# Performance work log

Hardware: AMD Instinct MI355X
Metric: run time of the kernel (lower is better)

Reference implementation:

```python
import jax, jax.numpy as jnp
import numpy as np

B, N_IN, N_OPS, E = 2048, 64, 1024, 64   # graphs, leaf inputs, operations, embed_size
N_OIO, N_TIO, VOCAB = 4, 4, 1000         # one-input ops, two-input ops, embedding rows


def setup_inputs() -> dict:
    key = jax.random.key(0)
    ks = jax.random.split(key, 8)
    rng = np.random.default_rng(0)
    # random valid DAG topology: op j may read any node with index < N_IN + j
    op_kind = rng.integers(0, 2, N_OPS)
    t_oio = rng.integers(0, N_OIO, N_OPS)
    t_tio = rng.integers(0, N_TIO, N_OPS)
    op_w_idx = np.where(op_kind == 0, t_oio, N_OIO + t_tio).astype(np.int32)
    op_in1 = np.array([rng.integers(0, N_IN + j) for j in range(N_OPS)], dtype=np.int32)
    op_in2 = np.array([rng.integers(0, N_IN + j) for j in range(N_OPS)], dtype=np.int32)
    s = 0.1  # keep relu chain numerically tame
    return {
        "input_ids": jax.random.randint(ks[0], (B, N_IN), 0, VOCAB, dtype=jnp.int32),
        "op_w_idx": jnp.asarray(op_w_idx),
        "op_in1": jnp.asarray(op_in1),
        "op_in2": jnp.asarray(op_in2),
        "embedding": jax.random.normal(ks[1], (VOCAB, E), jnp.float32) * s,
        "oio_W": jax.random.normal(ks[2], (N_OIO, E, E), jnp.float32) * s,
        "oio_b": jax.random.normal(ks[3], (N_OIO, E), jnp.float32) * s,
        "tio_W": jax.random.normal(ks[4], (N_TIO, 2 * E, E), jnp.float32) * s,
        "tio_b": jax.random.normal(ks[5], (N_TIO, E), jnp.float32) * s,
        "final_W": jax.random.normal(ks[6], (E, 1), jnp.float32) * s,
        "final_b": jax.random.normal(ks[7], (1,), jnp.float32) * s,
    }


def reference(input_ids, op_w_idx, op_in1, op_in2, embedding,
              oio_W, oio_b, tio_W, tio_b, final_W, final_b):
    # Unify weights: one-input Linear(E,E) padded with zeros on the x2 half,
    # so cat(x1, x2) @ W_pad + b == x1 @ W + b (identical math to the torch module).
    W_all = jnp.concatenate(
        [jnp.concatenate([oio_W, jnp.zeros_like(oio_W)], axis=1), tio_W], axis=0)  # (8, 2E, E)
    b_all = jnp.concatenate([oio_b, tio_b], axis=0)                                # (8, E)

    leaves = embedding[input_ids]                                   # (B, N_IN, E)
    nodes0 = jnp.concatenate(
        [leaves, jnp.zeros((B, N_OPS, E), leaves.dtype)], axis=1)   # (B, N_IN+N_OPS, E)

    def step(nodes, op):
        j, widx, i1, i2 = op
        x1 = jnp.take(nodes, i1, axis=1)                            # (B, E)
        x2 = jnp.take(nodes, i2, axis=1)                            # (B, E)
        h = jax.nn.relu(jnp.concatenate([x1, x2], axis=-1) @ W_all[widx] + b_all[widx])
        nodes = jax.lax.dynamic_update_slice(nodes, h[:, None, :], (0, N_IN + j, 0))
        return nodes, None

    xs = (jnp.arange(N_OPS, dtype=jnp.int32), op_w_idx, op_in1, op_in2)
    nodes, _ = jax.lax.scan(step, nodes0, xs)

    # operation_counter: final Linear(E, 1) on the last produced node tensor
    return nodes[:, -1, :] @ final_W + final_b                      # (B, 1)
```

## Files before the change

### kernel.cpp

```cpp
#include <hip/hip_runtime.h>

#define NIN 64
#define NOPS 1024
#define NB 2048
#define NNODES 1088
#define SLAB_SH 18

#define WS_SCHED 0u
#define WS_LEV   8192u
#define WS_WT    16384u
#define WS_BIAS  147456u
#define WS_NODES 163840u

#define LM_LINES 0u
#define LM_SCHED 65536u
#define LM_MSTA  73728u
#define LM_TOTAL 77824u

typedef unsigned int u32;
typedef unsigned short u16;
typedef unsigned long long u64;
typedef _Float16 f16;
typedef _Float16 f16x8 __attribute__((ext_vector_type(8)));
typedef _Float16 f16x4 __attribute__((ext_vector_type(4)));
typedef float f32x4 __attribute__((ext_vector_type(4)));

#define MFMA16(a, b, c) __builtin_amdgcn_mfma_f32_16x16x32_f16((a), (b), (c), 0, 0, 0)


__global__ __launch_bounds__(1024) void k_sched(const int* __restrict__ wxv,
                                                const int* __restrict__ in1v,
                                                const int* __restrict__ in2v,
                                                char* __restrict__ ws, int cap) {
  __shared__ int s1[NOPS], s2[NOPS], sw[NOPS], slv[NOPS];
  __shared__ int lcnt[132];
  __shared__ int cnt2[1032];
  __shared__ u64 s_pack[NOPS];
  __shared__ int dl[NNODES], slot_of[NNODES], stk[NNODES];
  __shared__ int opPos[NOPS];
  __shared__ unsigned char needG[NOPS];
  __shared__ int s_flag, s_nlev, s_top, s_next;
  const int j = threadIdx.x;
  s1[j] = in1v[j]; s2[j] = in2v[j]; sw[j] = wxv[j]; slv[j] = 1;
  needG[j] = 0;
  if (j < 132) lcnt[j] = 0;
  if (j < 1032) cnt2[j] = 0;
  __syncthreads();
  for (int it = 0; it < NOPS + 1; ++it) {
    if (j == 0) s_flag = 0;
    __syncthreads();
    int p1 = s1[j];
    int l1 = (p1 >= NIN) ? slv[p1 - NIN] : 0;
    int l2 = 0;
    if (sw[j] >= 4) { int p2 = s2[j]; l2 = (p2 >= NIN) ? slv[p2 - NIN] : 0; }
    int nl = 1 + (l1 > l2 ? l1 : l2);
    if (nl != slv[j]) { slv[j] = nl; s_flag = 1; }
    __syncthreads();
    int f = s_flag;
    __syncthreads();
    if (!f) break;
  }
  if (j == 0) s_nlev = 0;
  __syncthreads();
  atomicMax(&s_nlev, slv[j]);
  __syncthreads();
  u32* wl = (u32*)(ws + WS_LEV);
  const int nlev = s_nlev;
  if (nlev > 127) { if (j == 0) { wl[0] = 0; wl[1] = 0; wl[2] = 1; } return; }
  atomicAdd(&lcnt[slv[j]], 1);
  atomicAdd(&cnt2[slv[j] * 8 + sw[j]], 1);
  __syncthreads();
  if (j == 0) {
    int acc = 0;
    for (int L = 1; L <= nlev; ++L) { int c = lcnt[L]; lcnt[L] = acc; acc += c; }
  }
  __syncthreads();
  int base = -1;
  if (j >= 8 && j < (nlev + 1) * 8) {
    int L = j >> 3, mm = j & 7;
    int s = lcnt[L];
    for (int q = 0; q < mm; ++q) s += cnt2[L * 8 + q];
    base = s;
  }
  u16* msta = (u16*)(ws + WS_LEV + 4096);
  for (int t = j; t < 2048; t += 1024) msta[t] = (u16)NOPS;
  __syncthreads();
  if (base >= 0) { cnt2[j] = base; msta[j] = (u16)base; }
  __syncthreads();
  { int slot = atomicAdd(&cnt2[slv[j] * 8 + sw[j]], 1);
    u64 p = (u64)(u32)s1[j] | ((u64)(u32)s2[j] << 11) | ((u64)(u32)sw[j] << 22) | ((u64)(u32)j << 25);
    s_pack[slot] = p;
    opPos[j] = slot - lcnt[slv[j]]; }
  __syncthreads();
  if (j == NOPS - 1) needG[j] = 1;
  { int L = slv[j];
    int i1n = s1[j];
    if (i1n >= NIN) { int p = i1n - NIN; if (!(slv[p] == L - 1 && opPos[p] < 64)) needG[p] = 1; }
    if (sw[j] >= 4) {
      int i2n = s2[j];
      if (i2n >= NIN) { int p = i2n - NIN; if (!(slv[p] == L - 1 && opPos[p] < 64)) needG[p] = 1; }
    } }
  for (int t = j; t < NNODES; t += 1024) dl[t] = (t < NIN) ? 0 : slv[t - NIN];
  __syncthreads();
  atomicMax(&dl[s1[j]], slv[j]);
  if (sw[j] >= 4) atomicMax(&dl[s2[j]], slv[j]);
  __syncthreads();
  if (j == 0) { dl[NNODES - 1] = nlev + 1; s_top = 0; s_next = NIN; }
  if (j < NIN) slot_of[j] = j;
  __syncthreads();
  for (int L = 1; L <= nlev; ++L) {
    for (int t = j; t < NNODES; t += 1024)
      if (dl[t] == L - 1) { int p = atomicAdd(&s_top, 1); stk[p] = slot_of[t]; }
    __syncthreads();
    if (slv[j] == L) {
      int p = atomicSub(&s_top, 1);
      int s;
      if (p >= 1) s = stk[p - 1]; else s = atomicAdd(&s_next, 1);
      slot_of[NIN + j] = s;
    }
    __syncthreads();
    if (j == 0 && s_top < 0) s_top = 0;
    __syncthreads();
  }
  {
    u64 m = s_pack[j];
    int i1n = (int)(m & 2047u), i2n = (int)((m >> 11) & 2047u);
    u32 wxn = (u32)((m >> 22) & 7u);
    int opn = (int)((m >> 25) & 2047u);
    int Lop = slv[opn];
    int two = (wxn >= 4);
    if (!two) i2n = i1n;
    u32 f1 = 0, p1 = 0, f2 = 0, p2 = 0;
    if (i1n >= NIN) { int p = i1n - NIN;
      if (slv[p] == Lop - 1 && opPos[p] < 64) { f1 = 1; p1 = (u32)opPos[p]; } }
    if (i2n >= NIN) { int p = i2n - NIN;
      if (slv[p] == Lop - 1 && opPos[p] < 64) { f2 = 1; p2 = (u32)opPos[p]; } }
    u32 op_pos = (u32)opPos[opn];
    u32 ldsout = (op_pos < 64) ? 1u : 0u;
    u32 gout   = needG[opn] ? 1u : 0u;
    u32 s1slot = (u32)slot_of[i1n];
    u32 s2slot = (u32)slot_of[i2n];
    u64 nm = (u64)s1slot | ((u64)s2slot << 11) | ((u64)wxn << 22)
           | ((u64)(u32)slot_of[NIN + opn] << 25)
           | ((u64)p1 << 36) | ((u64)f1 << 43)
           | ((u64)p2 << 44) | ((u64)f2 << 51)
           | ((u64)(op_pos & 63u) << 52) | ((u64)ldsout << 59)
           | ((u64)gout << 60);
    ((u64*)(ws + WS_SCHED))[j] = nm;
  }
  if (j == 0) {
    wl[0] = (u32)nlev;
    wl[1] = (u32)slot_of[NNODES - 1];
    wl[2] = (s_next > cap) ? 1u : 0u;
  }
}

__global__ __launch_bounds__(256) void k_weights(const float* __restrict__ oW,
                                                 const float* __restrict__ ob,
                                                 const float* __restrict__ tW,
                                                 const float* __restrict__ tb,
                                                 char* __restrict__ ws) {
  f16* wt = (f16*)(ws + WS_WT);
  int t = blockIdx.x * 256 + threadIdx.x;
  #pragma unroll
  for (int q = 0; q < 4; ++q) {
    int e = t * 4 + q;
    int mat = e >> 13, n = (e >> 7) & 63, k = e & 127;
    float v;
    if (mat < 4) v = (k < 64) ? oW[mat * 4096 + k * 64 + n] : 0.f;
    else         v = tW[(mat - 4) * 8192 + k * 64 + n];
    wt[e] = (f16)v;
  }
  if (blockIdx.x == 0) {
    float* bs = (float*)(ws + WS_BIAS);
    for (int q = threadIdx.x; q < 512; q += 256)
      bs[q] = (q < 256) ? ob[q] : tb[q - 256];
  }
}

__global__ __launch_bounds__(256) void k_leaves(const int* __restrict__ ids,
                                                const float* __restrict__ emb,
                                                char* __restrict__ ws) {
  int p = blockIdx.x * 256 + threadIdx.x;
  int i = p >> 11, b = p & 2047;
  int id = ids[b * 64 + i];
  const f32x4* src = (const f32x4*)(emb + (u32)id * 64u);
  f16x8* dst = (f16x8*)(ws + WS_NODES + ((u32)i << SLAB_SH) + (u32)b * 128u);
  #pragma unroll
  for (int q = 0; q < 8; ++q) {
    f32x4 lo = src[2 * q], hi = src[2 * q + 1];
    f16x8 v = { (f16)lo.x, (f16)lo.y, (f16)lo.z, (f16)lo.w,
                (f16)hi.x, (f16)hi.y, (f16)hi.z, (f16)hi.w };
    dst[q] = v;
  }
}

__global__ __launch_bounds__(512, 4) void k_main(char* __restrict__ ws) {
  extern __shared__ char lds[];
  const int tid = threadIdx.x;
  const u32* wl = (const u32*)(ws + WS_LEV);
  if (wl[2]) return;
  for (int t = tid; t < NOPS; t += 512)
    ((u64*)(lds + LM_SCHED))[t] = ((const u64*)(ws + WS_SCHED))[t];
  for (int t = tid; t < 1024; t += 512)
    ((u32*)(lds + LM_MSTA))[t] = ((const u32*)(ws + WS_LEV + 4096))[t];
  const int nlev = (int)wl[0];

  const int lane   = tid & 63;
  const int m      = tid >> 6;
  const int lhi    = lane >> 4, llo = lane & 15;
  const int op_sub = llo >> 2;
  const int brow   = llo & 3;
  const int r0     = blockIdx.x * 4;
  char* nodes = ws + WS_NODES;

  const f16* wp = (const f16*)(ws + WS_WT) + m * 8192 + llo * 128 + lhi * 8;
  const f16x8 W00 = *(const f16x8*)(wp +        0), W01 = *(const f16x8*)(wp +       32),
              W10 = *(const f16x8*)(wp + 2048 + 0), W11 = *(const f16x8*)(wp + 2048 + 32),
              W20 = *(const f16x8*)(wp + 4096 + 0), W21 = *(const f16x8*)(wp + 4096 + 32),
              W30 = *(const f16x8*)(wp + 6144 + 0), W31 = *(const f16x8*)(wp + 6144 + 32);
  f16x8 W02 = {}, W03 = {}, W12 = {}, W13 = {}, W22 = {}, W23 = {}, W32 = {}, W33 = {};
  if (m >= 4) {
    W02 = *(const f16x8*)(wp +        64); W03 = *(const f16x8*)(wp +        96);
    W12 = *(const f16x8*)(wp + 2048 + 64); W13 = *(const f16x8*)(wp + 2048 + 96);
    W22 = *(const f16x8*)(wp + 4096 + 64); W23 = *(const f16x8*)(wp + 4096 + 96);
    W32 = *(const f16x8*)(wp + 6144 + 64); W33 = *(const f16x8*)(wp + 6144 + 96);
  }
  const float* bsp = (const float*)(ws + WS_BIAS) + m * 64 + lhi * 4;
  const f32x4 B0 = *(const f32x4*)(bsp),      B1 = *(const f32x4*)(bsp + 16),
              B2 = *(const f32x4*)(bsp + 32), B3 = *(const f32x4*)(bsp + 48);
  __syncthreads();

  const u64* s_sched = (const u64*)(lds + LM_SCHED);
  const u16* s_msta  = (const u16*)(lds + LM_MSTA);

  const u32 a_off  = (u32)((r0 + brow) * 128 + lhi * 16);
  const u32 st_off = (u32)((r0 + brow) * 128 + lhi * 8);
  const u32 key   = (u32)(brow << 4);
  const u32 aL0   = (u32)(brow * 128 + ((lhi * 16)      ^ key));
  const u32 aL1   = (u32)(brow * 128 + ((lhi * 16 + 64) ^ key));
  const u32 stL0  = (u32)(brow * 128 + ((      lhi * 8) ^ key));
  const u32 stL1  = (u32)(brow * 128 + (( 32 + lhi * 8) ^ key));
  const u32 stL2  = (u32)(brow * 128 + (( 64 + lhi * 8) ^ key));
  const u32 stL3  = (u32)(brow * 128 + (( 96 + lhi * 8) ^ key));

  for (int L = 1; L <= nlev; ++L) {
    const u32 rb = (u32)(((L - 1) & 1) << 15);
    const u32 wb = (u32)((L & 1) << 15);
    int k0 = (int)s_msta[L * 8 + m];
    int k1 = (int)s_msta[L * 8 + m + 1];
    k0 = __builtin_amdgcn_readfirstlane(k0);
    k1 = __builtin_amdgcn_readfirstlane(k1);
    const int ke = k1 - 1;
    for (int g = k0; g < k1; g += 4) {
      int kop = g + op_sub; kop = kop > ke ? ke : kop;
      u64 md = s_sched[kop];
      f16x8 a0, a1;
      if ((md >> 43) & 1) {
        const char* l1 = lds + rb + (((u32)(md >> 36) & 63u) << 9);
        a0 = *(const f16x8*)(l1 + aL0);
        a1 = *(const f16x8*)(l1 + aL1);
      } else {
        const char* b1 = nodes + ((u64)((u32)md & 2047u) << SLAB_SH) + a_off;
        a0 = *(const f16x8*)(b1);
        a1 = *(const f16x8*)(b1 + 64);
      }
      f16x8 a2 = {}, a3 = {};
      if (m >= 4) {
        if ((md >> 51) & 1) {
          const char* l2 = lds + rb + (((u32)(md >> 44) & 63u) << 9);
          a2 = *(const f16x8*)(l2 + aL0);
          a3 = *(const f16x8*)(l2 + aL1);
        } else {
          const char* b2 = nodes + ((u64)(((u32)(md >> 11)) & 2047u) << SLAB_SH) + a_off;
          a2 = *(const f16x8*)(b2);
          a3 = *(const f16x8*)(b2 + 64);
        }
      }
      f32x4 c0 = B0, c1 = B1, c2 = B2, c3 = B3;
      __builtin_amdgcn_s_setprio(1);
      c0 = MFMA16(W00, a0, c0); c0 = MFMA16(W01, a1, c0);
      c1 = MFMA16(W10, a0, c1); c1 = MFMA16(W11, a1, c1);
      c2 = MFMA16(W20, a0, c2); c2 = MFMA16(W21, a1, c2);
      c3 = MFMA16(W30, a0, c3); c3 = MFMA16(W31, a1, c3);
      if (m >= 4) {
        c0 = MFMA16(W02, a2, c0); c0 = MFMA16(W03, a3, c0);
        c1 = MFMA16(W12, a2, c1); c1 = MFMA16(W13, a3, c1);
        c2 = MFMA16(W22, a2, c2); c2 = MFMA16(W23, a3, c2);
        c3 = MFMA16(W32, a2, c3); c3 = MFMA16(W33, a3, c3);
      }
      __builtin_amdgcn_s_setprio(0);
      f16x4 r0v = { (f16)(c0.x > 0.f ? c0.x : 0.f), (f16)(c0.y > 0.f ? c0.y : 0.f),
                    (f16)(c0.z > 0.f ? c0.z : 0.f), (f16)(c0.w > 0.f ? c0.w : 0.f) };
      f16x4 r1v = { (f16)(c1.x > 0.f ? c1.x : 0.f), (f16)(c1.y > 0.f ? c1.y : 0.f),
                    (f16)(c1.z > 0.f ? c1.z : 0.f), (f16)(c1.w > 0.f ? c1.w : 0.f) };
      f16x4 r2v = { (f16)(c2.x > 0.f ? c2.x : 0.f), (f16)(c2.y > 0.f ? c2.y : 0.f),
                    (f16)(c2.z > 0.f ? c2.z : 0.f), (f16)(c2.w > 0.f ? c2.w : 0.f) };
      f16x4 r3v = { (f16)(c3.x > 0.f ? c3.x : 0.f), (f16)(c3.y > 0.f ? c3.y : 0.f),
                    (f16)(c3.z > 0.f ? c3.z : 0.f), (f16)(c3.w > 0.f ? c3.w : 0.f) };
      if ((md >> 59) & 1) {
        char* lp = lds + wb + (((u32)(md >> 52) & 63u) << 9);
        *(f16x4*)(lp + stL0) = r0v;
        *(f16x4*)(lp + stL1) = r1v;
        *(f16x4*)(lp + stL2) = r2v;
        *(f16x4*)(lp + stL3) = r3v;
      }
      if ((md >> 60) & 1) {
        char* st = nodes + (((u64)((md >> 25) & 2047u)) << SLAB_SH) + st_off;
        *(f16x4*)(st)      = r0v;
        *(f16x4*)(st + 32) = r1v;
        *(f16x4*)(st + 64) = r2v;
        *(f16x4*)(st + 96) = r3v;
      }
    }
    __syncthreads();
  }
}

__global__ __launch_bounds__(256) void k_final(const float* __restrict__ fw,
                                               const float* __restrict__ fb,
                                               const char* __restrict__ ws,
                                               float* __restrict__ out) {
  __shared__ float s_fw[64];
  int t = threadIdx.x;
  if (t < 64) s_fw[t] = fw[t];
  __syncthreads();
  int b = blockIdx.x * 256 + t;
  const u32* wl = (const u32*)(ws + WS_LEV);
  if (wl[2]) { out[b] = 0.f; return; }
  u32 slot = wl[1];
  const f16x8* last = (const f16x8*)(ws + WS_NODES + ((u64)slot << SLAB_SH) + (u32)b * 128u);
  float acc = fb[0];
  #pragma unroll
  for (int q = 0; q < 8; ++q) {
    f16x8 v = last[q];
    #pragma unroll
    for (int e = 0; e < 8; ++e) acc += (float)v[e] * s_fw[q * 8 + e];
  }
  out[b] = acc;
}

extern "C" void kernel_launch(void* const* d_in, const int* in_sizes, int n_in,
                              void* d_out, int out_size, void* d_ws, size_t ws_size,
                              hipStream_t stream) {
  const int*   ids = (const int*)d_in[0];
  const int*   wx  = (const int*)d_in[1];
  const int*   i1  = (const int*)d_in[2];
  const int*   i2  = (const int*)d_in[3];
  const float* emb = (const float*)d_in[4];
  const float* oW  = (const float*)d_in[5];
  const float* ob  = (const float*)d_in[6];
  const float* tW  = (const float*)d_in[7];
  const float* tb  = (const float*)d_in[8];
  const float* fw  = (const float*)d_in[9];
  const float* fb  = (const float*)d_in[10];
  char* ws = (char*)d_ws;
  float* out = (float*)d_out;

  int cap = (int)((ws_size > (size_t)WS_NODES) ? ((ws_size - WS_NODES) >> SLAB_SH) : 0);
  if (cap < 80) return;
  if (cap > 2047) cap = 2047;

  hipLaunchKernelGGL(k_sched,   dim3(1),   dim3(1024), 0, stream, wx, i1, i2, ws, cap);
  hipLaunchKernelGGL(k_weights, dim3(64),  dim3(256),  0, stream, oW, ob, tW, tb, ws);
  hipLaunchKernelGGL(k_leaves,  dim3(512), dim3(256),  0, stream, ids, emb, ws);
  hipLaunchKernelGGL(k_main,    dim3(512), dim3(512),  LM_TOTAL, stream, ws);
  hipLaunchKernelGGL(k_final,   dim3(8),   dim3(256),  0, stream, fw, fb, ws, out);
}
```

Before: 124.0 us.

## Trim scheduler barriers, merge prep kernels, re-swizzle LDS and pin weight registers

The level-assignment loop drops from three barriers per iteration to one by rotating among three flag slots. The slot allocator's stack is pre-filled with free slots, which removes the fallback counter and one barrier per level. The weight-conversion and leaf-embedding kernels are merged into a single prep launch to save a launch. In the main kernel, the LDS swizzle also XORs in the op position to spread bank accesses, and empty asm statements keep the weight fragments in VGPRs. These changes add complexity to the allocator's error handling.

```diff
diff --git a/kernel.cpp b/kernel.cpp
--- a/kernel.cpp
+++ b/kernel.cpp
@@ -36,32 +36,32 @@
   __shared__ int lcnt[132];
   __shared__ int cnt2[1032];
   __shared__ u64 s_pack[NOPS];
-  __shared__ int dl[NNODES], slot_of[NNODES], stk[NNODES];
+  __shared__ int dl[NNODES], slot_of[NNODES];
+  __shared__ int stk[2304];
   __shared__ int opPos[NOPS];
   __shared__ unsigned char needG[NOPS];
-  __shared__ int s_flag, s_nlev, s_top, s_next;
+  __shared__ int s_flags[3];
+  __shared__ int s_nlev, s_top, s_err;
   const int j = threadIdx.x;
   s1[j] = in1v[j]; s2[j] = in2v[j]; sw[j] = wxv[j]; slv[j] = 1;
   needG[j] = 0;
   if (j < 132) lcnt[j] = 0;
   if (j < 1032) cnt2[j] = 0;
+  if (j < 3) s_flags[j] = 0;
+  if (j == 0) { s_nlev = 0; s_err = 0; }
   __syncthreads();
   for (int it = 0; it < NOPS + 1; ++it) {
-    if (j == 0) s_flag = 0;
-    __syncthreads();
+    int c = it % 3;
     int p1 = s1[j];
     int l1 = (p1 >= NIN) ? slv[p1 - NIN] : 0;
     int l2 = 0;
     if (sw[j] >= 4) { int p2 = s2[j]; l2 = (p2 >= NIN) ? slv[p2 - NIN] : 0; }
     int nl = 1 + (l1 > l2 ? l1 : l2);
-    if (nl != slv[j]) { slv[j] = nl; s_flag = 1; }
+    if (nl != slv[j]) { slv[j] = nl; s_flags[c] = 1; }
+    if (j == 0) s_flags[(it + 1) % 3] = 0;
     __syncthreads();
-    int f = s_flag;
-    __syncthreads();
-    if (!f) break;
-  }
-  if (j == 0) s_nlev = 0;
-  __syncthreads();
+    if (!s_flags[c]) break;
+  }
   atomicMax(&s_nlev, slv[j]);
   __syncthreads();
   u32* wl = (u32*)(ws + WS_LEV);
@@ -105,21 +105,25 @@
   atomicMax(&dl[s1[j]], slv[j]);
   if (sw[j] >= 4) atomicMax(&dl[s2[j]], slv[j]);
   __syncthreads();
-  if (j == 0) { dl[NNODES - 1] = nlev + 1; s_top = 0; s_next = NIN; }
+  if (j == 0) dl[NNODES - 1] = nlev + 1;
   if (j < NIN) slot_of[j] = j;
+  { int S = cap - 64; if (S > 1152) S = 1152;
+    for (int t = j; t < S; t += 1024) stk[t] = 64 + t;
+    if (j == 0) s_top = S; }
   __syncthreads();
   for (int L = 1; L <= nlev; ++L) {
     for (int t = j; t < NNODES; t += 1024)
-      if (dl[t] == L - 1) { int p = atomicAdd(&s_top, 1); stk[p] = slot_of[t]; }
+      if (dl[t] == L - 1) {
+        int p = atomicAdd(&s_top, 1);
+        if (p >= 0 && p < 2304) stk[p] = slot_of[t];
+      }
     __syncthreads();
     if (slv[j] == L) {
       int p = atomicSub(&s_top, 1);
       int s;
-      if (p >= 1) s = stk[p - 1]; else s = atomicAdd(&s_next, 1);
+      if (p >= 1) s = stk[p - 1]; else { s = 64; s_err = 1; }
       slot_of[NIN + j] = s;
     }
-    __syncthreads();
-    if (j == 0 && s_top < 0) s_top = 0;
     __syncthreads();
   }
   {
@@ -151,36 +155,17 @@
   if (j == 0) {
     wl[0] = (u32)nlev;
     wl[1] = (u32)slot_of[NNODES - 1];
-    wl[2] = (s_next > cap) ? 1u : 0u;
-  }
-}
-
-__global__ __launch_bounds__(256) void k_weights(const float* __restrict__ oW,
-                                                 const float* __restrict__ ob,
-                                                 const float* __restrict__ tW,
-                                                 const float* __restrict__ tb,
-                                                 char* __restrict__ ws) {
-  f16* wt = (f16*)(ws + WS_WT);
-  int t = blockIdx.x * 256 + threadIdx.x;
-  #pragma unroll
-  for (int q = 0; q < 4; ++q) {
-    int e = t * 4 + q;
-    int mat = e >> 13, n = (e >> 7) & 63, k = e & 127;
-    float v;
-    if (mat < 4) v = (k < 64) ? oW[mat * 4096 + k * 64 + n] : 0.f;
-    else         v = tW[(mat - 4) * 8192 + k * 64 + n];
-    wt[e] = (f16)v;
-  }
-  if (blockIdx.x == 0) {
-    float* bs = (float*)(ws + WS_BIAS);
-    for (int q = threadIdx.x; q < 512; q += 256)
-      bs[q] = (q < 256) ? ob[q] : tb[q - 256];
-  }
-}
-
-__global__ __launch_bounds__(256) void k_leaves(const int* __restrict__ ids,
-                                                const float* __restrict__ emb,
-                                                char* __restrict__ ws) {
+    wl[2] = s_err ? 1u : 0u;
+  }
+}
+
+__global__ __launch_bounds__(256) void k_prep(const int* __restrict__ ids,
+                                              const float* __restrict__ emb,
+                                              const float* __restrict__ oW,
+                                              const float* __restrict__ ob,
+                                              const float* __restrict__ tW,
+                                              const float* __restrict__ tb,
+                                              char* __restrict__ ws) {
   int p = blockIdx.x * 256 + threadIdx.x;
   int i = p >> 11, b = p & 2047;
   int id = ids[b * 64 + i];
@@ -193,6 +178,24 @@
                 (f16)hi.x, (f16)hi.y, (f16)hi.z, (f16)hi.w };
     dst[q] = v;
   }
+  if (blockIdx.x < 64) {
+    f16* wt = (f16*)(ws + WS_WT);
+    int t = blockIdx.x * 256 + threadIdx.x;
+    #pragma unroll
+    for (int q = 0; q < 4; ++q) {
+      int e = t * 4 + q;
+      int mat = e >> 13, n = (e >> 7) & 63, k = e & 127;
+      float v;
+      if (mat < 4) v = (k < 64) ? oW[mat * 4096 + k * 64 + n] : 0.f;
+      else         v = tW[(mat - 4) * 8192 + k * 64 + n];
+      wt[e] = (f16)v;
+    }
+    if (blockIdx.x == 0) {
+      float* bs = (float*)(ws + WS_BIAS);
+      for (int q = threadIdx.x; q < 512; q += 256)
+        bs[q] = (q < 256) ? ob[q] : tb[q - 256];
+    }
+  }
 }
 
 __global__ __launch_bounds__(512, 4) void k_main(char* __restrict__ ws) {
@@ -215,10 +218,10 @@
   char* nodes = ws + WS_NODES;
 
   const f16* wp = (const f16*)(ws + WS_WT) + m * 8192 + llo * 128 + lhi * 8;
-  const f16x8 W00 = *(const f16x8*)(wp +        0), W01 = *(const f16x8*)(wp +       32),
-              W10 = *(const f16x8*)(wp + 2048 + 0), W11 = *(const f16x8*)(wp + 2048 + 32),
-              W20 = *(const f16x8*)(wp + 4096 + 0), W21 = *(const f16x8*)(wp + 4096 + 32),
-              W30 = *(const f16x8*)(wp + 6144 + 0), W31 = *(const f16x8*)(wp + 6144 + 32);
+  f16x8 W00 = *(const f16x8*)(wp +        0), W01 = *(const f16x8*)(wp +       32),
+        W10 = *(const f16x8*)(wp + 2048 + 0), W11 = *(const f16x8*)(wp + 2048 + 32),
+        W20 = *(const f16x8*)(wp + 4096 + 0), W21 = *(const f16x8*)(wp + 4096 + 32),
+        W30 = *(const f16x8*)(wp + 6144 + 0), W31 = *(const f16x8*)(wp + 6144 + 32);
   f16x8 W02 = {}, W03 = {}, W12 = {}, W13 = {}, W22 = {}, W23 = {}, W32 = {}, W33 = {};
   if (m >= 4) {
     W02 = *(const f16x8*)(wp +        64); W03 = *(const f16x8*)(wp +        96);
@@ -226,6 +229,10 @@
     W22 = *(const f16x8*)(wp + 4096 + 64); W23 = *(const f16x8*)(wp + 4096 + 96);
     W32 = *(const f16x8*)(wp + 6144 + 64); W33 = *(const f16x8*)(wp + 6144 + 96);
   }
+  asm volatile("" : "+v"(W00), "+v"(W01), "+v"(W10), "+v"(W11),
+                    "+v"(W20), "+v"(W21), "+v"(W30), "+v"(W31));
+  asm volatile("" : "+v"(W02), "+v"(W03), "+v"(W12), "+v"(W13),
+                    "+v"(W22), "+v"(W23), "+v"(W32), "+v"(W33));
   const float* bsp = (const float*)(ws + WS_BIAS) + m * 64 + lhi * 4;
   const f32x4 B0 = *(const f32x4*)(bsp),      B1 = *(const f32x4*)(bsp + 16),
               B2 = *(const f32x4*)(bsp + 32), B3 = *(const f32x4*)(bsp + 48);
@@ -236,13 +243,14 @@
 
   const u32 a_off  = (u32)((r0 + brow) * 128 + lhi * 16);
   const u32 st_off = (u32)((r0 + brow) * 128 + lhi * 8);
-  const u32 key   = (u32)(brow << 4);
-  const u32 aL0   = (u32)(brow * 128 + ((lhi * 16)      ^ key));
-  const u32 aL1   = (u32)(brow * 128 + ((lhi * 16 + 64) ^ key));
-  const u32 stL0  = (u32)(brow * 128 + ((      lhi * 8) ^ key));
-  const u32 stL1  = (u32)(brow * 128 + (( 32 + lhi * 8) ^ key));
-  const u32 stL2  = (u32)(brow * 128 + (( 64 + lhi * 8) ^ key));
-  const u32 stL3  = (u32)(brow * 128 + (( 96 + lhi * 8) ^ key));
+  const u32 key  = (u32)(brow << 4);
+  const u32 bA   = (u32)(brow * 128);
+  const u32 cA0  = (u32)((lhi * 16)      ^ key);
+  const u32 cA1  = (u32)((lhi * 16 + 64) ^ key);
+  const u32 cS0  = (u32)((      lhi * 8) ^ key);
+  const u32 cS1  = (u32)(( 32 + lhi * 8) ^ key);
+  const u32 cS2  = (u32)(( 64 + lhi * 8) ^ key);
+  const u32 cS3  = (u32)(( 96 + lhi * 8) ^ key);
 
   for (int L = 1; L <= nlev; ++L) {
     const u32 rb = (u32)(((L - 1) & 1) << 15);
@@ -257,9 +265,11 @@
       u64 md = s_sched[kop];
       f16x8 a0, a1;
       if ((md >> 43) & 1) {
-        const char* l1 = lds + rb + (((u32)(md >> 36) & 63u) << 9);
-        a0 = *(const f16x8*)(l1 + aL0);
-        a1 = *(const f16x8*)(l1 + aL1);
+        u32 pos = (u32)(md >> 36) & 63u;
+        const char* l1 = lds + rb + (pos << 9);
+        u32 px = (pos & 3u) << 5;
+        a0 = *(const f16x8*)(l1 + bA + (cA0 ^ px));
+        a1 = *(const f16x8*)(l1 + bA + (cA1 ^ px));
       } else {
         const char* b1 = nodes + ((u64)((u32)md & 2047u) << SLAB_SH) + a_off;
         a0 = *(const f16x8*)(b1);
@@ -268,9 +278,11 @@
       f16x8 a2 = {}, a3 = {};
       if (m >= 4) {
         if ((md >> 51) & 1) {
-          const char* l2 = lds + rb + (((u32)(md >> 44) & 63u) << 9);
-          a2 = *(const f16x8*)(l2 + aL0);
-          a3 = *(const f16x8*)(l2 + aL1);
+          u32 pos = (u32)(md >> 44) & 63u;
+          const char* l2 = lds + rb + (pos << 9);
+          u32 px = (pos & 3u) << 5;
+          a2 = *(const f16x8*)(l2 + bA + (cA0 ^ px));
+          a3 = *(const f16x8*)(l2 + bA + (cA1 ^ px));
         } else {
           const char* b2 = nodes + ((u64)(((u32)(md >> 11)) & 2047u) << SLAB_SH) + a_off;
           a2 = *(const f16x8*)(b2);
@@ -299,11 +311,13 @@
       f16x4 r3v = { (f16)(c3.x > 0.f ? c3.x : 0.f), (f16)(c3.y > 0.f ? c3.y : 0.f),
                     (f16)(c3.z > 0.f ? c3.z : 0.f), (f16)(c3.w > 0.f ? c3.w : 0.f) };
       if ((md >> 59) & 1) {
-        char* lp = lds + wb + (((u32)(md >> 52) & 63u) << 9);
-        *(f16x4*)(lp + stL0) = r0v;
-        *(f16x4*)(lp + stL1) = r1v;
-        *(f16x4*)(lp + stL2) = r2v;
-        *(f16x4*)(lp + stL3) = r3v;
+        u32 opos = (u32)(md >> 52) & 63u;
+        char* lp = lds + wb + (opos << 9);
+        u32 px = (opos & 3u) << 5;
+        *(f16x4*)(lp + bA + (cS0 ^ px)) = r0v;
+        *(f16x4*)(lp + bA + (cS1 ^ px)) = r1v;
+        *(f16x4*)(lp + bA + (cS2 ^ px)) = r2v;
+        *(f16x4*)(lp + bA + (cS3 ^ px)) = r3v;
       }
       if ((md >> 60) & 1) {
         char* st = nodes + (((u64)((md >> 25) & 2047u)) << SLAB_SH) + st_off;
@@ -361,9 +375,8 @@
   if (cap < 80) return;
   if (cap > 2047) cap = 2047;
 
-  hipLaunchKernelGGL(k_sched,   dim3(1),   dim3(1024), 0, stream, wx, i1, i2, ws, cap);
-  hipLaunchKernelGGL(k_weights, dim3(64),  dim3(256),  0, stream, oW, ob, tW, tb, ws);
-  hipLaunchKernelGGL(k_leaves,  dim3(512), dim3(256),  0, stream, ids, emb, ws);
-  hipLaunchKernelGGL(k_main,    dim3(512), dim3(512),  LM_TOTAL, stream, ws);
-  hipLaunchKernelGGL(k_final,   dim3(8),   dim3(256),  0, stream, fw, fb, ws, out);
-}
+  hipLaunchKernelGGL(k_sched, dim3(1),   dim3(1024), 0, stream, wx, i1, i2, ws, cap);
+  hipLaunchKernelGGL(k_prep,  dim3(512), dim3(256),  0, stream, ids, emb, oW, ob, tW, tb, ws);
+  hipLaunchKernelGGL(k_main,  dim3(512), dim3(512),  LM_TOTAL, stream, ws);
+  hipLaunchKernelGGL(k_final, dim3(8),   dim3(256),  0, stream, fw, fb, ws, out);
+}
```

Measured after the change: 120.7 us. -2.6%, faster.
